# Kernel tuning notes

Hardware: AMD Instinct MI355X
Metric: run time of the kernel (lower is better)

Reference implementation:

```python
import jax, jax.numpy as jnp
import numpy as np

# Nominal per-type footprint heights used only to pick a STATIC scatter window
# (must upper-bound the node_size values produced in setup_inputs()).
_MAX_SX = {1: 1.0, 2: 1.0, 3: 1.0}
_MAX_SY = {1: 1.0, 2: 2.5, 3: 5.0}


def _raster(stm, t, sx, sy, width, height, nbx, nby):
    """Rasterize all sites of type t (each a sx-by-sy rect at integer (rw,cl))
    into an (nbx,nby) capacity histogram with fractional bin overlap."""
    binW = width / nbx
    binH = height / nby
    KX = int(np.ceil(_MAX_SX[t] / binW)) + 1  # static window of candidate bins in x
    KY = int(np.ceil(_MAX_SY[t] / binH)) + 1  # static window of candidate bins in y
    idx = jnp.arange(width * height, dtype=jnp.int32)
    r = (idx // height).astype(jnp.float32)  # site x coordinate (rw)
    c = (idx % height).astype(jnp.float32)   # site y coordinate (cl)
    mask = stm == t
    iLo = jnp.floor(r / binW).astype(jnp.int32)
    jLo = jnp.floor(c / binH).astype(jnp.int32)
    cap = jnp.zeros((nbx, nby), jnp.float32)
    for di in range(KX):
        i = iLo + di
        w = jnp.minimum((i + 1) * binW, r + sx) - jnp.maximum(i * binW, r)
        okx = (i <= nbx - 1) & (w > 0)
        ic = jnp.minimum(i, nbx - 1)
        for dj in range(KY):
            j = jLo + dj
            h = jnp.minimum((j + 1) * binH, c + sy) - jnp.maximum(j * binH, c)
            contrib = jnp.where(mask & okx & (j <= nby - 1) & (h > 0), w * h, 0.0)
            cap = cap.at[ic, jnp.minimum(j, nby - 1)].add(contrib)
    return cap


def setup_inputs() -> dict:
    key = jax.random.key(0)
    W = H = 2048
    NBX = NBY = 2048
    stm = jax.random.randint(key, (W * H,), 0, 4, dtype=jnp.int32)
    node_size_x = jnp.ones((4,), jnp.float32)                       # all site types 1 wide
    node_size_y = jnp.array([1.0, 1.0, 2.5, 5.0], jnp.float32)      # SLICE/SLICE/DSP/RAM heights
    return {
        "site_type_map": stm,
        "node_size_x": node_size_x,
        "node_size_y": node_size_y,
        "width": W, "height": H,
        "num_bins_x": NBX, "num_bins_y": NBY,
        "xl": 0, "xh": W, "yl": 0, "yh": H,
    }


def reference(site_type_map, node_size_x, node_size_y, width, height,
              num_bins_x, num_bins_y, xl, xh, yl, yh):
    cap0 = _raster(site_type_map, 1, node_size_x[0], node_size_y[0],
                   width, height, num_bins_x, num_bins_y)
    cap2 = _raster(site_type_map, 2, node_size_x[2], node_size_y[2],
                   width, height, num_bins_x, num_bins_y)
    cap3 = _raster(site_type_map, 3, node_size_x[3], node_size_y[3],
                   width, height, num_bins_x, num_bins_y)
    binArea = ((xh - xl) / num_bins_x) * ((yh - yl) / num_bins_y)
    # binCapMap1 aliases binCapMap0 in the torch code
    return (binArea - cap0, binArea - cap0, binArea - cap2, binArea - cap3)
```

## Files before the change

### kernel.cpp

```cpp
#include <hip/hip_runtime.h>


typedef float v4f __attribute__((ext_vector_type(4)));

__global__ __launch_bounds__(256) void demand_map_kernel(
    const int* __restrict__ stm,
    const float* __restrict__ nsx,
    const float* __restrict__ nsy,
    const int* __restrict__ heightP,
    const int* __restrict__ nbxP, const int* __restrict__ nbyP,
    const int* __restrict__ xlP, const int* __restrict__ xhP,
    const int* __restrict__ ylP, const int* __restrict__ yhP,
    float* __restrict__ out,
    int total)
{
    const int n4 = total >> 2;
    const int base = blockIdx.x * 512;
    const int g0 = base + threadIdx.x;
    const int g1 = g0 + 256;
    if (g0 >= n4) return;
    const bool do1 = (g1 < n4);

    const int height = *heightP;
    const float binArea =
        ((float)(*xhP - *xlP) / (float)(*nbxP)) *
        ((float)(*yhP - *ylP) / (float)(*nbyP));

    const float wx1 = fminf(nsx[0], 1.0f);
    const float wx2 = fminf(nsx[2], 1.0f);
    const float wx3 = fminf(nsx[3], 1.0f);
    const float sy1 = nsy[0], sy2 = nsy[2], sy3 = nsy[3];
    float w1[2], w2[4], w3[5];
    #pragma unroll
    for (int k = 0; k < 2; ++k) w1[k] = fminf(fmaxf(sy1 - (float)k, 0.0f), 1.0f);
    #pragma unroll
    for (int k = 0; k < 4; ++k) w2[k] = fminf(fmaxf(sy2 - (float)k, 0.0f), 1.0f);
    #pragma unroll
    for (int k = 0; k < 5; ++k) w3[k] = fminf(fmaxf(sy3 - (float)k, 0.0f), 1.0f);

    const int4* stm4 = (const int4*)stm;

    const int4 curA = stm4[g0];
    int4 prevA = make_int4(0, 0, 0, 0);
    if (((g0 << 2) % height) != 0) prevA = stm4[g0 - 1];
    int4 curB = make_int4(0, 0, 0, 0), prevB = make_int4(0, 0, 0, 0);
    if (do1) {
        curB = stm4[g1];
        if (((g1 << 2) % height) != 0) prevB = stm4[g1 - 1];
    }

    v4f* out4 = (v4f*)out;

    #pragma unroll
    for (int it = 0; it < 2; ++it) {
        if (it == 1 && !do1) break;
        const int g = (it == 0) ? g0 : g1;
        const int4 cur  = (it == 0) ? curA  : curB;
        const int4 prev = (it == 0) ? prevA : prevB;

        int s[8] = { prev.x, prev.y, prev.z, prev.w,
                     cur.x,  cur.y,  cur.z,  cur.w };

        float o0[4], o2[4], o3[4];
        #pragma unroll
        for (int e = 0; e < 4; ++e) {
            float c0 = w1[0] * (float)(s[4 + e] == 1)
                     + w1[1] * (float)(s[3 + e] == 1);
            float c2 = w2[0] * (float)(s[4 + e] == 2)
                     + w2[1] * (float)(s[3 + e] == 2)
                     + w2[2] * (float)(s[2 + e] == 2)
                     + w2[3] * (float)(s[1 + e] == 2);
            float c3 = w3[0] * (float)(s[4 + e] == 3)
                     + w3[1] * (float)(s[3 + e] == 3)
                     + w3[2] * (float)(s[2 + e] == 3)
                     + w3[3] * (float)(s[1 + e] == 3)
                     + w3[4] * (float)(s[0 + e] == 3);
            o0[e] = binArea - wx1 * c0;
            o2[e] = binArea - wx2 * c2;
            o3[e] = binArea - wx3 * c3;
        }

        const v4f v0 = { o0[0], o0[1], o0[2], o0[3] };
        const v4f v2 = { o2[0], o2[1], o2[2], o2[3] };
        const v4f v3 = { o3[0], o3[1], o3[2], o3[3] };
        __builtin_nontemporal_store(v0, &out4[g]);
        __builtin_nontemporal_store(v0, &out4[n4 + g]);
        __builtin_nontemporal_store(v2, &out4[2 * n4 + g]);
        __builtin_nontemporal_store(v3, &out4[3 * n4 + g]);
    }
}

extern "C" void kernel_launch(void* const* d_in, const int* in_sizes, int n_in,
                              void* d_out, int out_size, void* d_ws, size_t ws_size,
                              hipStream_t stream) {
    const int*   stm = (const int*)  d_in[0];
    const float* nsx = (const float*)d_in[1];
    const float* nsy = (const float*)d_in[2];
    const int* heightP = (const int*)d_in[4];
    const int* nbxP    = (const int*)d_in[5];
    const int* nbyP    = (const int*)d_in[6];
    const int* xlP     = (const int*)d_in[7];
    const int* xhP     = (const int*)d_in[8];
    const int* ylP     = (const int*)d_in[9];
    const int* yhP     = (const int*)d_in[10];

    float* out = (float*)d_out;
    const int total = in_sizes[0];
    const int n4 = total >> 2;
    const int blocks = (n4 + 511) / 512;

    demand_map_kernel<<<blocks, 256, 0, stream>>>(
        stm, nsx, nsy, heightP, nbxP, nbyP, xlP, xhP, ylP, yhP, out, total);
}
```

Before: 17.41 us.

## Assign each wavefront one output map instead of all four per thread

Each block now covers 128 int4 groups, and each of its four wavefronts writes one of the four output maps. The per-thread work drops to a single 5-tap stencil and one store per iteration, where it used to compute three stencils and issue four stores. In exchange every input element is loaded four times, once per wavefront, which relies on cache hits, and the grid has four times as many blocks.

```diff
diff --git a/kernel.cpp b/kernel.cpp
--- a/kernel.cpp
+++ b/kernel.cpp
@@ -14,10 +14,12 @@
     float* __restrict__ out,
     int total)
 {
-    const int n4 = total >> 2;
-    const int base = blockIdx.x * 512;
-    const int g0 = base + threadIdx.x;
-    const int g1 = g0 + 256;
+    const int n4   = total >> 2;
+    const int wid  = threadIdx.x >> 6;
+    const int lane = threadIdx.x & 63;
+    const int base = blockIdx.x * 128;
+    const int g0 = base + lane;
+    const int g1 = g0 + 64;
     if (g0 >= n4) return;
     const bool do1 = (g1 < n4);
 
@@ -26,17 +28,13 @@
         ((float)(*xhP - *xlP) / (float)(*nbxP)) *
         ((float)(*yhP - *ylP) / (float)(*nbyP));
 
-    const float wx1 = fminf(nsx[0], 1.0f);
-    const float wx2 = fminf(nsx[2], 1.0f);
-    const float wx3 = fminf(nsx[3], 1.0f);
-    const float sy1 = nsy[0], sy2 = nsy[2], sy3 = nsy[3];
-    float w1[2], w2[4], w3[5];
+    const int t    = (wid <= 1) ? 1 : wid;
+    const int sidx = (wid <= 1) ? 0 : wid;
+    const float wx = fminf(nsx[sidx], 1.0f);
+    const float sy = nsy[sidx];
+    float w[5];
     #pragma unroll
-    for (int k = 0; k < 2; ++k) w1[k] = fminf(fmaxf(sy1 - (float)k, 0.0f), 1.0f);
-    #pragma unroll
-    for (int k = 0; k < 4; ++k) w2[k] = fminf(fmaxf(sy2 - (float)k, 0.0f), 1.0f);
-    #pragma unroll
-    for (int k = 0; k < 5; ++k) w3[k] = fminf(fmaxf(sy3 - (float)k, 0.0f), 1.0f);
+    for (int k = 0; k < 5; ++k) w[k] = fminf(fmaxf(sy - (float)k, 0.0f), 1.0f);
 
     const int4* stm4 = (const int4*)stm;
 
@@ -50,6 +48,7 @@
     }
 
     v4f* out4 = (v4f*)out;
+    const int mapOff = wid * n4;
 
     #pragma unroll
     for (int it = 0; it < 2; ++it) {
@@ -61,32 +60,18 @@
         int s[8] = { prev.x, prev.y, prev.z, prev.w,
                      cur.x,  cur.y,  cur.z,  cur.w };
 
-        float o0[4], o2[4], o3[4];
+        float o[4];
         #pragma unroll
         for (int e = 0; e < 4; ++e) {
-            float c0 = w1[0] * (float)(s[4 + e] == 1)
-                     + w1[1] * (float)(s[3 + e] == 1);
-            float c2 = w2[0] * (float)(s[4 + e] == 2)
-                     + w2[1] * (float)(s[3 + e] == 2)
-                     + w2[2] * (float)(s[2 + e] == 2)
-                     + w2[3] * (float)(s[1 + e] == 2);
-            float c3 = w3[0] * (float)(s[4 + e] == 3)
-                     + w3[1] * (float)(s[3 + e] == 3)
-                     + w3[2] * (float)(s[2 + e] == 3)
-                     + w3[3] * (float)(s[1 + e] == 3)
-                     + w3[4] * (float)(s[0 + e] == 3);
-            o0[e] = binArea - wx1 * c0;
-            o2[e] = binArea - wx2 * c2;
-            o3[e] = binArea - wx3 * c3;
+            float c = 0.0f;
+            #pragma unroll
+            for (int k = 0; k < 5; ++k)
+                c += w[k] * (float)(s[4 + e - k] == t);
+            o[e] = binArea - wx * c;
         }
 
-        const v4f v0 = { o0[0], o0[1], o0[2], o0[3] };
-        const v4f v2 = { o2[0], o2[1], o2[2], o2[3] };
-        const v4f v3 = { o3[0], o3[1], o3[2], o3[3] };
-        __builtin_nontemporal_store(v0, &out4[g]);
-        __builtin_nontemporal_store(v0, &out4[n4 + g]);
-        __builtin_nontemporal_store(v2, &out4[2 * n4 + g]);
-        __builtin_nontemporal_store(v3, &out4[3 * n4 + g]);
+        const v4f v = { o[0], o[1], o[2], o[3] };
+        __builtin_nontemporal_store(v, &out4[mapOff + g]);
     }
 }
 
@@ -107,7 +92,7 @@
     float* out = (float*)d_out;
     const int total = in_sizes[0];
     const int n4 = total >> 2;
-    const int blocks = (n4 + 511) / 512;
+    const int blocks = (n4 + 127) / 128;
 
     demand_map_kernel<<<blocks, 256, 0, stream>>>(
         stm, nsx, nsy, heightP, nbxP, nbyP, xlP, xhP, ylP, yhP, out, total);
```

New measurement: 18.40 us. +5.7%, slower.
